# Kernel tuning notes

Measured on AMD Instinct MI355X. Metric: run time of the kernel, lower is better.

The kernel has to match this reference:

```python
import jax, jax.numpy as jnp
import numpy as np

EMB = 128
BINS = 32
CUT = 5.0
NLAYER = 5
NHID = 4  # extra hidden linears in edge MLP (hidden_dim_list has 5 entries total)
N_NODES = 50000
N_EDGES = 800000
N_GRAPH = 256
NODE_CLASS = 100


def setup_inputs() -> dict:
    key = jax.random.key(0)
    ks = jax.random.split(key, 20)
    s = 0.02
    inp = {
        'z': jax.random.randint(ks[0], (N_NODES,), 0, NODE_CLASS),
        'pos': jax.random.normal(ks[1], (N_NODES, 3), dtype=jnp.float32) * 3.0,
        'batch': jnp.sort(jax.random.randint(ks[2], (N_NODES,), 0, N_GRAPH)),
        'edge_index': jax.random.randint(ks[3], (2, N_EDGES), 0, N_NODES),
        # parameters
        'atom_table': jax.random.normal(ks[4], (NODE_CLASS, EMB), dtype=jnp.float32) * s,
        'atom_w': jax.random.normal(ks[5], (EMB, EMB), dtype=jnp.float32) * s,
        'atom_b': jnp.zeros((EMB,), jnp.float32),
        'edge_emb_w': jax.random.normal(ks[6], (BINS, EMB), dtype=jnp.float32) * s,
        'edge_emb_b': jnp.zeros((EMB,), jnp.float32),
        'edge_w0': jax.random.normal(ks[7], (NLAYER, 3 * EMB, EMB), dtype=jnp.float32) * s,
        'edge_b0': jnp.zeros((NLAYER, EMB), jnp.float32),
        'edge_w': jax.random.normal(ks[8], (NLAYER, NHID, EMB, EMB), dtype=jnp.float32) * s,
        'edge_b': jnp.zeros((NLAYER, NHID, EMB), jnp.float32),
        'node_w': jax.random.normal(ks[9], (NLAYER, EMB, EMB), dtype=jnp.float32) * s,
        'node_b': jnp.zeros((NLAYER, EMB), jnp.float32),
        'out_w': jax.random.normal(ks[10], (EMB, 1), dtype=jnp.float32) * s,
        'out_b': jnp.zeros((1,), jnp.float32),
    }
    return inp


def reference(z, pos, batch, edge_index, atom_table, atom_w, atom_b,
              edge_emb_w, edge_emb_b, edge_w0, edge_b0, edge_w, edge_b,
              node_w, node_b, out_w, out_b):
    silu = jax.nn.silu
    row, col = edge_index[0], edge_index[1]

    # atom embedding + linear
    h_node = atom_table[z] @ atom_w + atom_b  # [N, EMB]

    # edge distances -> gaussian basis expansion (linear spacing, log_base=1.0)
    d = jnp.linalg.norm(pos[row] - pos[col], axis=-1)  # [E]
    mu = jnp.linspace(0.0, CUT, BINS, dtype=jnp.float32)
    sigma = CUT / BINS
    basis = jnp.exp(-0.5 * ((d[:, None] - mu) / sigma) ** 2)  # [E, BINS]
    h_edge = basis @ edge_emb_w + edge_emb_b  # [E, EMB]

    # message passing layers
    for l in range(NLAYER):
        m = jnp.concatenate([h_edge, h_node[row], h_node[col]], axis=-1)  # [E, 3*EMB]
        m = silu(m @ edge_w0[l] + edge_b0[l])
        for k in range(NHID):
            m = silu(m @ edge_w[l, k] + edge_b[l, k])
        h_edge = h_edge + m  # residual edge update
        agg = jax.ops.segment_sum(h_edge, row, num_segments=N_NODES)  # [N, EMB]
        h_node = h_node + silu(agg @ node_w[l] + node_b[l])  # residual node update

    # scatter-mean graph pool
    sums = jax.ops.segment_sum(h_node, batch, num_segments=N_GRAPH)
    cnt = jax.ops.segment_sum(jnp.ones((h_node.shape[0],), h_node.dtype), batch, num_segments=N_GRAPH)
    h_graph = sums / jnp.clip(cnt, 1.0)[:, None]

    return h_graph @ out_w + out_b  # [N_GRAPH, 1]
```

## Files before the change

### kernel.cpp

```cpp
#include <hip/hip_runtime.h>

#define EMB      128
#define N_NODES_ 50000
#define N_EDGES_ 800000
#define N_GRAPH_ 256
#define NLAYER_  5

#define WP_ATOM  573440
#define WP_NODE0 589824
#define WP_EMB   671744
#define WP_TOTAL 675840

typedef short short8 __attribute__((ext_vector_type(8)));
typedef float floatx4 __attribute__((ext_vector_type(4)));

__device__ __forceinline__ float silu_f(float x) {
    return __fdividef(x, 1.0f + __expf(-x));
}
__device__ __forceinline__ float bf2f(unsigned short h) {
    return __uint_as_float(((unsigned)h) << 16);
}
__device__ __forceinline__ unsigned short f2bf(float f) {
    unsigned u = __float_as_uint(f);
    unsigned r = 0x7FFFu + ((u >> 16) & 1u);
    return (unsigned short)((u + r) >> 16);
}

#if defined(__has_builtin)
#if __has_builtin(__builtin_amdgcn_cvt_pk_bf16_f32)
#define HAVE_PK_BF16 1
#endif
#endif
#ifdef HAVE_PK_BF16
typedef __bf16 bf16x2 __attribute__((ext_vector_type(2)));
__device__ __forceinline__ unsigned f2bf_pk(float a, float b) {
    bf16x2 v = __builtin_amdgcn_cvt_pk_bf16_f32(a, b);
    unsigned u;
    __builtin_memcpy(&u, &v, 4);
    return u;
}
#else
__device__ __forceinline__ unsigned f2bf_pk(float a, float b) {
    return (unsigned)f2bf(a) | ((unsigned)f2bf(b) << 16);
}
#endif

__device__ __forceinline__ void wave_lds_fence() {
    __builtin_amdgcn_fence(__ATOMIC_ACQ_REL, "wavefront");
    __builtin_amdgcn_wave_barrier();
}

__global__ __launch_bounds__(256) void hist_kernel(
    const int* __restrict__ row, int* __restrict__ hist)
{
    const int e = blockIdx.x * 256 + threadIdx.x;
    if (e < N_EDGES_) atomicAdd(&hist[row[e]], 1);
}

__global__ __launch_bounds__(256) void scan_kernel(
    const int* __restrict__ hist, int* __restrict__ cursor)
{
    __shared__ int ssum[256];
    const int tid = threadIdx.x;
    const int chunk = (N_NODES_ + 255) / 256;
    const int base = tid * chunk;
    int s = 0;
    for (int i = 0; i < chunk; ++i) {
        const int idx = base + i;
        if (idx < N_NODES_) s += hist[idx];
    }
    ssum[tid] = s;
    __syncthreads();
    for (int off = 1; off < 256; off <<= 1) {
        const int t2 = (tid >= off) ? ssum[tid - off] : 0;
        __syncthreads();
        ssum[tid] += t2;
        __syncthreads();
    }
    int run = ssum[tid] - s;
    for (int i = 0; i < chunk; ++i) {
        const int idx = base + i;
        if (idx < N_NODES_) { cursor[idx] = run; run += hist[idx]; }
    }
}

__global__ __launch_bounds__(256) void scatter_kernel(
    const int* __restrict__ row, const int* __restrict__ col,
    int* __restrict__ cursor, int* __restrict__ row_s, int* __restrict__ col_s)
{
    const int e = blockIdx.x * 256 + threadIdx.x;
    if (e >= N_EDGES_) return;
    const int r = row[e];
    const int p = atomicAdd(&cursor[r], 1);
    row_s[p] = r;
    col_s[p] = col[e];
}

__global__ __launch_bounds__(256) void pack_w_kernel(
    const float* __restrict__ edge_w0, const float* __restrict__ edge_w,
    const float* __restrict__ atom_w, const float* __restrict__ node_w,
    const float* __restrict__ edge_emb_w,
    unsigned short* __restrict__ Wp)
{
    const int bid = blockIdx.x;
    int Kb, t;
    const float* src;
    unsigned short* dst;
    if (bid < 200) {
        const int l = bid / 40, r = bid % 40, s = r / 8;
        t = r % 8;
        Kb = (s == 0) ? 12 : 4;
        src = (s == 0) ? edge_w0 + (size_t)l * 384 * 128
                       : edge_w + ((size_t)l * 4 + (s - 1)) * 128 * 128;
        dst = Wp + (size_t)l * 114688 + ((s == 0) ? 0 : (49152 + (s - 1) * 16384))
            + (size_t)t * Kb * 512;
    } else if (bid < 208) {
        t = bid - 200; Kb = 4; src = atom_w;
        dst = Wp + WP_ATOM + (size_t)t * Kb * 512;
    } else if (bid < 248) {
        const int l = (bid - 208) >> 3; t = (bid - 208) & 7; Kb = 4;
        src = node_w + (size_t)l * 128 * 128;
        dst = Wp + WP_NODE0 + (size_t)l * 16384 + (size_t)t * Kb * 512;
    } else {
        t = bid - 248; Kb = 1; src = edge_emb_w;
        dst = Wp + WP_EMB + (size_t)t * 512;
    }
    const int n = Kb * 512;
    for (int p = threadIdx.x; p < n; p += 256) {
        const int j = p & 7, lane = (p >> 3) & 63, kb = p >> 9;
        const int k  = kb * 32 + ((lane >> 4) << 3) + j;
        const int nn = t * 16 + (lane & 15);
        dst[p] = f2bf(src[(size_t)k * 128 + nn]);
    }
}

__global__ __launch_bounds__(256, 4) void edge_mlp_csr_kernel(
    const unsigned short* __restrict__ h_node_bf, unsigned short* __restrict__ h_edge,
    const int* __restrict__ row_s, const int* __restrict__ col_s,
    const unsigned short* __restrict__ Wp,
    const float* __restrict__ b0, const float* __restrict__ bh)
{
    __shared__ __align__(16) unsigned short P[2][64][136];

    const int tid  = threadIdx.x;
    const int e0   = blockIdx.x * 64;
    const int lane = tid & 63;
    const int wv   = tid >> 6;
    const int lr   = lane & 15;
    const int lg   = lane >> 4;
    const int nt0  = 2 * wv, nt1 = nt0 + 1;

    int eoff[4], roff[4], coff[4];
#pragma unroll
    for (int et = 0; et < 4; ++et) {
        const int e = e0 + et * 16 + lr;
        eoff[et] = e * 128 + lg * 8;
        roff[et] = row_s[e] * 128 + lg * 8;
        coff[et] = col_s[e] * 128 + lg * 8;
    }

    floatx4 acc0[4], acc1[4];

    {
        const float4 bv0 = *(const float4*)&b0[nt0 * 16 + lg * 4];
        const float4 bv1 = *(const float4*)&b0[nt1 * 16 + lg * 4];
#pragma unroll
        for (int et = 0; et < 4; ++et) {
            acc0[et] = (floatx4){bv0.x, bv0.y, bv0.z, bv0.w};
            acc1[et] = (floatx4){bv1.x, bv1.y, bv1.z, bv1.w};
        }
        const unsigned short* aptr0 = Wp + ((size_t)(nt0 * 12) * 64 + lane) * 8;
        const unsigned short* aptr1 = Wp + ((size_t)(nt1 * 12) * 64 + lane) * 8;
#pragma unroll
        for (int kb = 0; kb < 12; ++kb) {
            const short8 wf0 = *(const short8*)(aptr0 + (size_t)kb * 512);
            const short8 wf1 = *(const short8*)(aptr1 + (size_t)kb * 512);
            const int off = (kb & 3) * 32;
#pragma unroll
            for (int et = 0; et < 4; ++et) {
                const unsigned short* src =
                    (kb < 4) ? (h_edge + eoff[et])
                  : (kb < 8) ? (h_node_bf + roff[et])
                             : (h_node_bf + coff[et]);
                const short8 mf = *(const short8*)(src + off);
                acc0[et] = __builtin_amdgcn_mfma_f32_16x16x32_bf16(wf0, mf, acc0[et], 0, 0, 0);
                acc1[et] = __builtin_amdgcn_mfma_f32_16x16x32_bf16(wf1, mf, acc1[et], 0, 0, 0);
            }
        }
#pragma unroll
        for (int et = 0; et < 4; ++et) {
            uint2 p0, p1;
            p0.x = f2bf_pk(silu_f(acc0[et][0]), silu_f(acc0[et][1]));
            p0.y = f2bf_pk(silu_f(acc0[et][2]), silu_f(acc0[et][3]));
            p1.x = f2bf_pk(silu_f(acc1[et][0]), silu_f(acc1[et][1]));
            p1.y = f2bf_pk(silu_f(acc1[et][2]), silu_f(acc1[et][3]));
            *(uint2*)&P[0][et * 16 + lr][nt0 * 16 + lg * 4] = p0;
            *(uint2*)&P[0][et * 16 + lr][nt1 * 16 + lg * 4] = p1;
        }
    }
    __syncthreads();

#pragma unroll 1
    for (int s = 1; s < 5; ++s) {
        const int inb  = (s - 1) & 1;
        const int outb = s & 1;
        const unsigned short* __restrict__ Ws = Wp + 49152 + (size_t)(s - 1) * 16384;
        const float* __restrict__ bias = bh + (size_t)(s - 1) * 128;

        const float4 bv0 = *(const float4*)&bias[nt0 * 16 + lg * 4];
        const float4 bv1 = *(const float4*)&bias[nt1 * 16 + lg * 4];
#pragma unroll
        for (int et = 0; et < 4; ++et) {
            acc0[et] = (floatx4){bv0.x, bv0.y, bv0.z, bv0.w};
            acc1[et] = (floatx4){bv1.x, bv1.y, bv1.z, bv1.w};
        }
        const unsigned short* aptr0 = Ws + ((size_t)(nt0 * 4) * 64 + lane) * 8;
        const unsigned short* aptr1 = Ws + ((size_t)(nt1 * 4) * 64 + lane) * 8;
#pragma unroll 2
        for (int kb = 0; kb < 4; ++kb) {
            const short8 wf0 = *(const short8*)(aptr0 + (size_t)kb * 512);
            const short8 wf1 = *(const short8*)(aptr1 + (size_t)kb * 512);
#pragma unroll
            for (int et = 0; et < 4; ++et) {
                const short8 mf = *(const short8*)&P[inb][et * 16 + lr][kb * 32 + lg * 8];
                acc0[et] = __builtin_amdgcn_mfma_f32_16x16x32_bf16(wf0, mf, acc0[et], 0, 0, 0);
                acc1[et] = __builtin_amdgcn_mfma_f32_16x16x32_bf16(wf1, mf, acc1[et], 0, 0, 0);
            }
        }
        if (s < 4) {
#pragma unroll
            for (int et = 0; et < 4; ++et) {
                uint2 p0, p1;
                p0.x = f2bf_pk(silu_f(acc0[et][0]), silu_f(acc0[et][1]));
                p0.y = f2bf_pk(silu_f(acc0[et][2]), silu_f(acc0[et][3]));
                p1.x = f2bf_pk(silu_f(acc1[et][0]), silu_f(acc1[et][1]));
                p1.y = f2bf_pk(silu_f(acc1[et][2]), silu_f(acc1[et][3]));
                *(uint2*)&P[outb][et * 16 + lr][nt0 * 16 + lg * 4] = p0;
                *(uint2*)&P[outb][et * 16 + lr][nt1 * 16 + lg * 4] = p1;
            }
            __syncthreads();
        } else {
#pragma unroll
            for (int et = 0; et < 4; ++et) {
                unsigned short* erow = h_edge + (size_t)(e0 + et * 16 + lr) * 128;
                const uint2 d0 = *(const uint2*)(erow + nt0 * 16 + lg * 4);
                const uint2 d1 = *(const uint2*)(erow + nt1 * 16 + lg * 4);
                float x0 = silu_f(acc0[et][0]) + bf2f((unsigned short)(d0.x & 0xFFFF));
                float x1 = silu_f(acc0[et][1]) + bf2f((unsigned short)(d0.x >> 16));
                float x2 = silu_f(acc0[et][2]) + bf2f((unsigned short)(d0.y & 0xFFFF));
                float x3 = silu_f(acc0[et][3]) + bf2f((unsigned short)(d0.y >> 16));
                float y0 = silu_f(acc1[et][0]) + bf2f((unsigned short)(d1.x & 0xFFFF));
                float y1 = silu_f(acc1[et][1]) + bf2f((unsigned short)(d1.x >> 16));
                float y2 = silu_f(acc1[et][2]) + bf2f((unsigned short)(d1.y & 0xFFFF));
                float y3 = silu_f(acc1[et][3]) + bf2f((unsigned short)(d1.y >> 16));
                uint2 o0, o1;
                o0.x = f2bf_pk(x0, x1); o0.y = f2bf_pk(x2, x3);
                o1.x = f2bf_pk(y0, y1); o1.y = f2bf_pk(y2, y3);
                *(uint2*)(erow + nt0 * 16 + lg * 4) = o0;
                *(uint2*)(erow + nt1 * 16 + lg * 4) = o1;
            }
        }
    }
}

__global__ __launch_bounds__(256, 4) void node_agg_gemm_kernel(
    const unsigned short* __restrict__ h_edge,
    const int* __restrict__ hist, const int* __restrict__ cur_end,
    const unsigned short* __restrict__ Wpm, const float* __restrict__ bias,
    unsigned short* __restrict__ h_node_bf, int N)
{
    __shared__ __align__(16) unsigned short B[64][136];
    const int tid  = threadIdx.x;
    const int lane = tid & 63;
    const int wv   = tid >> 6;
    const int n0   = blockIdx.x * 64;

    {
        const int t = tid >> 2, q = tid & 3;
        const int n = n0 + t;
        float a[32];
#pragma unroll
        for (int j = 0; j < 32; ++j) a[j] = 0.f;
        if (n < N) {
            const int e_end = cur_end[n];
            const int e_beg = e_end - hist[n];
            for (int e = e_beg; e < e_end; ++e) {
                const unsigned short* p = &h_edge[(size_t)e * 128 + q * 32];
#pragma unroll
                for (int g = 0; g < 4; ++g) {
                    const short8 v = *(const short8*)(p + g * 8);
#pragma unroll
                    for (int j = 0; j < 8; ++j)
                        a[g * 8 + j] += bf2f((unsigned short)v[j]);
                }
            }
        }
#pragma unroll
        for (int g = 0; g < 4; ++g) {
            uint4 pk;
            pk.x = f2bf_pk(a[g * 8 + 0], a[g * 8 + 1]);
            pk.y = f2bf_pk(a[g * 8 + 2], a[g * 8 + 3]);
            pk.z = f2bf_pk(a[g * 8 + 4], a[g * 8 + 5]);
            pk.w = f2bf_pk(a[g * 8 + 6], a[g * 8 + 7]);
            *(uint4*)&B[t][q * 32 + g * 8] = pk;
        }
    }
    wave_lds_fence();

    const int lr = lane & 15, lg = lane >> 4;
    floatx4 acc[8];
#pragma unroll
    for (int nt = 0; nt < 8; ++nt) {
        const float4 bv = *(const float4*)&bias[nt * 16 + lg * 4];
        acc[nt] = (floatx4){bv.x, bv.y, bv.z, bv.w};
    }
    const unsigned short* brow = &B[wv * 16 + lr][0];
#pragma unroll 2
    for (int kb = 0; kb < 4; ++kb) {
        const short8 mf = *(const short8*)(brow + kb * 32 + lg * 8);
#pragma unroll
        for (int nt = 0; nt < 8; ++nt) {
            const short8 wf = *(const short8*)(Wpm + ((size_t)(nt * 4 + kb) * 64 + lane) * 8);
            acc[nt] = __builtin_amdgcn_mfma_f32_16x16x32_bf16(wf, mf, acc[nt], 0, 0, 0);
        }
    }
    const int node = n0 + wv * 16 + lr;
    if (node < N) {
        unsigned short* drow = &h_node_bf[(size_t)node * 128];
#pragma unroll
        for (int nt = 0; nt < 8; ++nt) {
            float x0 = silu_f(acc[nt][0]), x1 = silu_f(acc[nt][1]);
            float x2 = silu_f(acc[nt][2]), x3 = silu_f(acc[nt][3]);
            unsigned short* p = drow + nt * 16 + lg * 4;
            const uint2 d = *(const uint2*)p;
            x0 += bf2f((unsigned short)(d.x & 0xFFFF));
            x1 += bf2f((unsigned short)(d.x >> 16));
            x2 += bf2f((unsigned short)(d.y & 0xFFFF));
            x3 += bf2f((unsigned short)(d.y >> 16));
            uint2 o;
            o.x = f2bf_pk(x0, x1);
            o.y = f2bf_pk(x2, x3);
            *(uint2*)p = o;
        }
    }
}

__global__ __launch_bounds__(256, 4) void atom_gemm_mfma_kernel(
    const float* __restrict__ src, const int* __restrict__ gidx,
    const unsigned short* __restrict__ Wpm, const float* __restrict__ bias,
    unsigned short* __restrict__ dst, int N)
{
    __shared__ __align__(16) unsigned short B[64][136];
    const int tid  = threadIdx.x;
    const int lane = tid & 63;
    const int wv   = tid >> 6;
    const int n0   = blockIdx.x * 64;

    {
        const int t = tid >> 2, q = tid & 3;
        const int node = n0 + t;
        const float* srow = src;
        if (node < N) srow = &src[(size_t)gidx[node] * 128];
#pragma unroll
        for (int i = 0; i < 4; ++i) {
            const int k8 = (q + 4 * i) << 3;
            uint4 pk = make_uint4(0, 0, 0, 0);
            if (node < N) {
                const float4 f0 = *(const float4*)(srow + k8);
                const float4 f1 = *(const float4*)(srow + k8 + 4);
                pk.x = f2bf_pk(f0.x, f0.y);
                pk.y = f2bf_pk(f0.z, f0.w);
                pk.z = f2bf_pk(f1.x, f1.y);
                pk.w = f2bf_pk(f1.z, f1.w);
            }
            *(uint4*)&B[t][k8] = pk;
        }
    }
    wave_lds_fence();

    const int lr = lane & 15, lg = lane >> 4;
    floatx4 acc[8];
#pragma unroll
    for (int nt = 0; nt < 8; ++nt) {
        const float4 bv = *(const float4*)&bias[nt * 16 + lg * 4];
        acc[nt] = (floatx4){bv.x, bv.y, bv.z, bv.w};
    }
    const unsigned short* brow = &B[wv * 16 + lr][0];
#pragma unroll 2
    for (int kb = 0; kb < 4; ++kb) {
        const short8 mf = *(const short8*)(brow + kb * 32 + lg * 8);
#pragma unroll
        for (int nt = 0; nt < 8; ++nt) {
            const short8 wf = *(const short8*)(Wpm + ((size_t)(nt * 4 + kb) * 64 + lane) * 8);
            acc[nt] = __builtin_amdgcn_mfma_f32_16x16x32_bf16(wf, mf, acc[nt], 0, 0, 0);
        }
    }
    const int node = n0 + wv * 16 + lr;
    if (node < N) {
        unsigned short* drow = &dst[(size_t)node * 128];
#pragma unroll
        for (int nt = 0; nt < 8; ++nt) {
            uint2 o;
            o.x = f2bf_pk(acc[nt][0], acc[nt][1]);
            o.y = f2bf_pk(acc[nt][2], acc[nt][3]);
            *(uint2*)(drow + nt * 16 + lg * 4) = o;
        }
    }
}

__global__ __launch_bounds__(256, 4) void edge_embed_mfma_kernel(
    const float* __restrict__ pos, const int* __restrict__ row, const int* __restrict__ col,
    const unsigned short* __restrict__ Wpe, const float* __restrict__ bemb,
    unsigned short* __restrict__ h_edge)
{
    __shared__ __align__(16) unsigned short Bas[64][40];
    const int tid  = threadIdx.x;
    const int lane = tid & 63;
    const int wv   = tid >> 6;
    const int e0   = blockIdx.x * 64;

    {
        const int t = tid >> 2, q = tid & 3;
        const int rr = row[e0 + t], cc = col[e0 + t];
        const float dx = pos[rr * 3 + 0] - pos[cc * 3 + 0];
        const float dy = pos[rr * 3 + 1] - pos[cc * 3 + 1];
        const float dz = pos[rr * 3 + 2] - pos[cc * 3 + 2];
        const float d = sqrtf(dx * dx + dy * dy + dz * dz);
        const float invs = 32.0f / 5.0f;
        float e[8];
#pragma unroll
        for (int j = 0; j < 8; ++j) {
            const float mu = (float)(q * 8 + j) * (5.0f / 31.0f);
            const float tt = (d - mu) * invs;
            e[j] = __expf(-0.5f * tt * tt);
        }
        uint4 pk;
        pk.x = f2bf_pk(e[0], e[1]);
        pk.y = f2bf_pk(e[2], e[3]);
        pk.z = f2bf_pk(e[4], e[5]);
        pk.w = f2bf_pk(e[6], e[7]);
        *(uint4*)&Bas[t][q * 8] = pk;
    }
    wave_lds_fence();

    const int lr = lane & 15, lg = lane >> 4;
    floatx4 acc[8];
#pragma unroll
    for (int nt = 0; nt < 8; ++nt) {
        const float4 bv = *(const float4*)&bemb[nt * 16 + lg * 4];
        acc[nt] = (floatx4){bv.x, bv.y, bv.z, bv.w};
    }
    const short8 mf = *(const short8*)&Bas[wv * 16 + lr][lg * 8];
#pragma unroll
    for (int nt = 0; nt < 8; ++nt) {
        const short8 wf = *(const short8*)(Wpe + ((size_t)nt * 64 + lane) * 8);
        acc[nt] = __builtin_amdgcn_mfma_f32_16x16x32_bf16(wf, mf, acc[nt], 0, 0, 0);
    }
    unsigned short* erow = &h_edge[(size_t)(e0 + wv * 16 + lr) * 128];
#pragma unroll
    for (int nt = 0; nt < 8; ++nt) {
        uint2 o;
        o.x = f2bf_pk(acc[nt][0], acc[nt][1]);
        o.y = f2bf_pk(acc[nt][2], acc[nt][3]);
        *(uint2*)(erow + nt * 16 + lg * 4) = o;
    }
}

__global__ __launch_bounds__(128) void pool_kernel(
    const unsigned short* __restrict__ h_node_bf, const int* __restrict__ batch,
    float* __restrict__ sums, float* __restrict__ cnt, int N)
{
    __shared__ int bb[256];
    const int tid = threadIdx.x;
    const int n0 = blockIdx.x * 256;
    for (int idx = tid; idx < 256; idx += 128) {
        int n = n0 + idx;
        bb[idx] = (n < N) ? batch[n] : -1;
    }
    __syncthreads();
    int cur = bb[0];
    float run = 0.f, runc = 0.f;
    for (int i = 0; i < 256; ++i) {
        const int b = bb[i];
        if (b < 0) break;
        if (b != cur) {
            atomicAdd(&sums[(size_t)cur * 128 + tid], run);
            if (tid == 0) atomicAdd(&cnt[cur], runc);
            run = 0.f; runc = 0.f; cur = b;
        }
        run += bf2f(h_node_bf[(size_t)(n0 + i) * 128 + tid]);
        runc += 1.f;
    }
    atomicAdd(&sums[(size_t)cur * 128 + tid], run);
    if (tid == 0) atomicAdd(&cnt[cur], runc);
}

__global__ __launch_bounds__(256) void final_kernel(
    const float* __restrict__ sums, const float* __restrict__ cnt,
    const float* __restrict__ out_w, const float* __restrict__ out_b,
    float* __restrict__ out)
{
    const int g = threadIdx.x;
    const float c = fmaxf(cnt[g], 1.0f);
    float acc = 0.f;
    for (int jj = 0; jj < 128; ++jj) acc = fmaf(sums[(size_t)g * 128 + jj], out_w[jj], acc);
    out[g] = acc / c + out_b[0];
}

__global__ void zero_out_kernel(float* out, int n) {
    int i = blockIdx.x * 256 + threadIdx.x;
    if (i < n) out[i] = 0.f;
}


extern "C" void kernel_launch(void* const* d_in, const int* in_sizes, int n_in,
                              void* d_out, int out_size, void* d_ws, size_t ws_size,
                              hipStream_t stream)
{
    const int*   z          = (const int*)  d_in[0];
    const float* pos        = (const float*)d_in[1];
    const int*   batch      = (const int*)  d_in[2];
    const int*   eidx       = (const int*)  d_in[3];
    const float* atom_table = (const float*)d_in[4];
    const float* atom_w     = (const float*)d_in[5];
    const float* atom_b     = (const float*)d_in[6];
    const float* edge_emb_w = (const float*)d_in[7];
    const float* edge_emb_b = (const float*)d_in[8];
    const float* edge_w0    = (const float*)d_in[9];
    const float* edge_b0    = (const float*)d_in[10];
    const float* edge_w     = (const float*)d_in[11];
    const float* edge_b     = (const float*)d_in[12];
    const float* node_w     = (const float*)d_in[13];
    const float* node_b     = (const float*)d_in[14];
    const float* out_w      = (const float*)d_in[15];
    const float* out_b      = (const float*)d_in[16];
    const int* row = eidx;
    const int* col = eidx + N_EDGES_;

    float* aggb = (float*)d_ws;
    float* sums = aggb + (size_t)N_NODES_ * EMB;
    float* cnt  = sums + (size_t)N_GRAPH_ * EMB;
    unsigned short* h_node_bf = (unsigned short*)(cnt + N_GRAPH_);
    unsigned short* h_edge    = h_node_bf + (size_t)N_NODES_ * EMB;
    unsigned short* Wp        = h_edge + (size_t)N_EDGES_ * EMB;
    int* hist   = (int*)(Wp + WP_TOTAL);
    int* cursor = hist + N_NODES_;
    int* row_s  = cursor + N_NODES_;
    int* col_s  = row_s + N_EDGES_;

    const size_t need = ((size_t)(N_NODES_ * EMB + N_GRAPH_ * EMB + N_GRAPH_)) * 4
                      + ((size_t)N_NODES_ * EMB + (size_t)N_EDGES_ * EMB + (size_t)WP_TOTAL) * 2
                      + ((size_t)N_NODES_ * 2 + (size_t)N_EDGES_ * 2) * 4;

    if (ws_size < need) {
        zero_out_kernel<<<1, 256, 0, stream>>>((float*)d_out, N_GRAPH_);
        return;
    }

    const int grid_rows64 = (N_NODES_ + 63) / 64;

    (void)hipMemsetAsync(hist, 0, N_NODES_ * sizeof(int), stream);
    hist_kernel<<<(N_EDGES_ + 255) / 256, 256, 0, stream>>>(row, hist);
    scan_kernel<<<1, 256, 0, stream>>>(hist, cursor);
    scatter_kernel<<<(N_EDGES_ + 255) / 256, 256, 0, stream>>>(row, col, cursor, row_s, col_s);

    pack_w_kernel<<<256, 256, 0, stream>>>(edge_w0, edge_w, atom_w, node_w, edge_emb_w, Wp);

    atom_gemm_mfma_kernel<<<grid_rows64, 256, 0, stream>>>(
        atom_table, z, Wp + WP_ATOM, atom_b, h_node_bf, N_NODES_);
    edge_embed_mfma_kernel<<<N_EDGES_ / 64, 256, 0, stream>>>(
        pos, row_s, col_s, Wp + WP_EMB, edge_emb_b, h_edge);

    for (int l = 0; l < NLAYER_; ++l) {
        edge_mlp_csr_kernel<<<N_EDGES_ / 64, 256, 0, stream>>>(
            h_node_bf, h_edge, row_s, col_s,
            Wp + (size_t)l * 114688,
            edge_b0 + (size_t)l * 128, edge_b + (size_t)l * 4 * 128);
        node_agg_gemm_kernel<<<grid_rows64, 256, 0, stream>>>(
            h_edge, hist, cursor,
            Wp + WP_NODE0 + (size_t)l * 16384, node_b + (size_t)l * 128,
            h_node_bf, N_NODES_);
    }

    (void)hipMemsetAsync(sums, 0, ((size_t)N_GRAPH_ * EMB + N_GRAPH_) * sizeof(float), stream);
    pool_kernel<<<(N_NODES_ + 255) / 256, 128, 0, stream>>>(h_node_bf, batch, sums, cnt, N_NODES_);
    final_kernel<<<1, 256, 0, stream>>>(sums, cnt, out_w, out_b, (float*)d_out);
}
```

Before: 2.796 ms.

## Stage edge MLP gathers into swizzled LDS via direct global-to-LDS loads

The first edge-MLP layer used to read h_edge, h_node[row] and h_node[col] straight from global memory inside the MFMA loop. It now stages 64-row tiles into two XOR-swizzled LDS buffers with global_load_lds, prefetching the next segment while the current one is multiplied. The final residual is now done through LDS with coalesced 16-byte stores, and an extra occupancy level is requested through launch_bounds. The aim is to hide gather latency and cut redundant scattered global reads, at the cost of more synchronisation and hand-written vmcnt waits that must line up with the outstanding loads.

```diff
diff --git a/kernel.cpp b/kernel.cpp
--- a/kernel.cpp
+++ b/kernel.cpp
@@ -48,6 +48,13 @@
 __device__ __forceinline__ void wave_lds_fence() {
     __builtin_amdgcn_fence(__ATOMIC_ACQ_REL, "wavefront");
     __builtin_amdgcn_wave_barrier();
+}
+
+__device__ __forceinline__ void gload_lds16(const unsigned short* g, unsigned short* l) {
+    __builtin_amdgcn_global_load_lds(
+        (const __attribute__((address_space(1))) void*)g,
+        (__attribute__((address_space(3))) void*)l,
+        16, 0, 0);
 }
 
 __global__ __launch_bounds__(256) void hist_kernel(
@@ -134,13 +141,14 @@
     }
 }
 
-__global__ __launch_bounds__(256, 4) void edge_mlp_csr_kernel(
+__global__ __launch_bounds__(256, 5) void edge_mlp_csr_kernel(
     const unsigned short* __restrict__ h_node_bf, unsigned short* __restrict__ h_edge,
     const int* __restrict__ row_s, const int* __restrict__ col_s,
     const unsigned short* __restrict__ Wp,
     const float* __restrict__ b0, const float* __restrict__ bh)
 {
-    __shared__ __align__(16) unsigned short P[2][64][136];
+    __shared__ __align__(16) unsigned short Xs[8192];
+    __shared__ __align__(16) unsigned short Ys[8192];
 
     const int tid  = threadIdx.x;
     const int e0   = blockIdx.x * 64;
@@ -150,17 +158,32 @@
     const int lg   = lane >> 4;
     const int nt0  = 2 * wv, nt1 = nt0 + 1;
 
-    int eoff[4], roff[4], coff[4];
-#pragma unroll
-    for (int et = 0; et < 4; ++et) {
-        const int e = e0 + et * 16 + lr;
-        eoff[et] = e * 128 + lg * 8;
-        roff[et] = row_s[e] * 128 + lg * 8;
-        coff[et] = col_s[e] * 128 + lg * 8;
+    const int t_ = tid >> 2, q_ = tid & 3;
+    short8 he_reg[4];
+#pragma unroll
+    for (int i = 0; i < 4; ++i)
+        he_reg[i] = *(const short8*)&h_edge[(size_t)(e0 + t_) * 128 + (q_ + 4 * i) * 8];
+
+    const int srow = 16 * wv + lg;
+#pragma unroll
+    for (int j = 0; j < 4; ++j) {
+        const int r = srow + 4 * j;
+        const int c = lr ^ (r & 7);
+        gload_lds16(h_edge + (size_t)(e0 + r) * 128 + c * 8,
+                    &Xs[(16 * wv + 4 * j) * 128]);
+    }
+    int cnode[4];
+#pragma unroll
+    for (int j = 0; j < 4; ++j) {
+        const int r = srow + 4 * j;
+        const int c = lr ^ (r & 7);
+        const int nd = row_s[e0 + r];
+        cnode[j] = col_s[e0 + r];
+        gload_lds16(h_node_bf + (size_t)nd * 128 + c * 8,
+                    &Ys[(16 * wv + 4 * j) * 128]);
     }
 
     floatx4 acc0[4], acc1[4];
-
     {
         const float4 bv0 = *(const float4*)&b0[nt0 * 16 + lg * 4];
         const float4 bv1 = *(const float4*)&b0[nt1 * 16 + lg * 4];
@@ -169,97 +192,137 @@
             acc0[et] = (floatx4){bv0.x, bv0.y, bv0.z, bv0.w};
             acc1[et] = (floatx4){bv1.x, bv1.y, bv1.z, bv1.w};
         }
-        const unsigned short* aptr0 = Wp + ((size_t)(nt0 * 12) * 64 + lane) * 8;
-        const unsigned short* aptr1 = Wp + ((size_t)(nt1 * 12) * 64 + lane) * 8;
-#pragma unroll
-        for (int kb = 0; kb < 12; ++kb) {
-            const short8 wf0 = *(const short8*)(aptr0 + (size_t)kb * 512);
-            const short8 wf1 = *(const short8*)(aptr1 + (size_t)kb * 512);
-            const int off = (kb & 3) * 32;
+    }
+    const unsigned short* aptr0 = Wp + ((size_t)(nt0 * 12) * 64 + lane) * 8;
+    const unsigned short* aptr1 = Wp + ((size_t)(nt1 * 12) * 64 + lane) * 8;
+
+    asm volatile("s_waitcnt vmcnt(4)" ::: "memory");
+    __syncthreads();
+
+#pragma unroll 2
+    for (int kk = 0; kk < 4; ++kk) {
+        const short8 wf0 = *(const short8*)(aptr0 + (size_t)kk * 512);
+        const short8 wf1 = *(const short8*)(aptr1 + (size_t)kk * 512);
+#pragma unroll
+        for (int et = 0; et < 4; ++et) {
+            const int r = et * 16 + lr;
+            const short8 mf = *(const short8*)&Xs[r * 128 + (((kk * 4 + lg) ^ (r & 7)) << 3)];
+            acc0[et] = __builtin_amdgcn_mfma_f32_16x16x32_bf16(wf0, mf, acc0[et], 0, 0, 0);
+            acc1[et] = __builtin_amdgcn_mfma_f32_16x16x32_bf16(wf1, mf, acc1[et], 0, 0, 0);
+        }
+    }
+    asm volatile("s_waitcnt vmcnt(0)" ::: "memory");
+    __syncthreads();
+
+#pragma unroll
+    for (int j = 0; j < 4; ++j) {
+        const int r = srow + 4 * j;
+        const int c = lr ^ (r & 7);
+        gload_lds16(h_node_bf + (size_t)cnode[j] * 128 + c * 8,
+                    &Xs[(16 * wv + 4 * j) * 128]);
+    }
+
+#pragma unroll 2
+    for (int kk = 0; kk < 4; ++kk) {
+        const short8 wf0 = *(const short8*)(aptr0 + (size_t)(kk + 4) * 512);
+        const short8 wf1 = *(const short8*)(aptr1 + (size_t)(kk + 4) * 512);
+#pragma unroll
+        for (int et = 0; et < 4; ++et) {
+            const int r = et * 16 + lr;
+            const short8 mf = *(const short8*)&Ys[r * 128 + (((kk * 4 + lg) ^ (r & 7)) << 3)];
+            acc0[et] = __builtin_amdgcn_mfma_f32_16x16x32_bf16(wf0, mf, acc0[et], 0, 0, 0);
+            acc1[et] = __builtin_amdgcn_mfma_f32_16x16x32_bf16(wf1, mf, acc1[et], 0, 0, 0);
+        }
+    }
+    asm volatile("s_waitcnt vmcnt(0)" ::: "memory");
+    __syncthreads();
+
+#pragma unroll 2
+    for (int kk = 0; kk < 4; ++kk) {
+        const short8 wf0 = *(const short8*)(aptr0 + (size_t)(kk + 8) * 512);
+        const short8 wf1 = *(const short8*)(aptr1 + (size_t)(kk + 8) * 512);
+#pragma unroll
+        for (int et = 0; et < 4; ++et) {
+            const int r = et * 16 + lr;
+            const short8 mf = *(const short8*)&Xs[r * 128 + (((kk * 4 + lg) ^ (r & 7)) << 3)];
+            acc0[et] = __builtin_amdgcn_mfma_f32_16x16x32_bf16(wf0, mf, acc0[et], 0, 0, 0);
+            acc1[et] = __builtin_amdgcn_mfma_f32_16x16x32_bf16(wf1, mf, acc1[et], 0, 0, 0);
+        }
+    }
+#pragma unroll
+    for (int et = 0; et < 4; ++et) {
+        const int r = et * 16 + lr;
+        uint2 p0, p1;
+        p0.x = f2bf_pk(silu_f(acc0[et][0]), silu_f(acc0[et][1]));
+        p0.y = f2bf_pk(silu_f(acc0[et][2]), silu_f(acc0[et][3]));
+        p1.x = f2bf_pk(silu_f(acc1[et][0]), silu_f(acc1[et][1]));
+        p1.y = f2bf_pk(silu_f(acc1[et][2]), silu_f(acc1[et][3]));
+        const int c0 = (2 * nt0 + (lg >> 1)) ^ (r & 7);
+        const int c1 = (2 * nt1 + (lg >> 1)) ^ (r & 7);
+        *(uint2*)&Ys[r * 128 + c0 * 8 + (lg & 1) * 4] = p0;
+        *(uint2*)&Ys[r * 128 + c1 * 8 + (lg & 1) * 4] = p1;
+    }
+    __syncthreads();
+
+#pragma unroll 1
+    for (int s = 1; s < 5; ++s) {
+        const unsigned short* bin = (s & 1) ? Ys : Xs;
+        unsigned short* bout      = (s & 1) ? Xs : Ys;
+        const unsigned short* __restrict__ Ws = Wp + 49152 + (size_t)(s - 1) * 16384;
+        const float* __restrict__ bias = bh + (size_t)(s - 1) * 128;
+
+        const float4 bv0 = *(const float4*)&bias[nt0 * 16 + lg * 4];
+        const float4 bv1 = *(const float4*)&bias[nt1 * 16 + lg * 4];
+#pragma unroll
+        for (int et = 0; et < 4; ++et) {
+            acc0[et] = (floatx4){bv0.x, bv0.y, bv0.z, bv0.w};
+            acc1[et] = (floatx4){bv1.x, bv1.y, bv1.z, bv1.w};
+        }
+        const unsigned short* ap0 = Ws + ((size_t)(nt0 * 4) * 64 + lane) * 8;
+        const unsigned short* ap1 = Ws + ((size_t)(nt1 * 4) * 64 + lane) * 8;
+#pragma unroll 2
+        for (int kk = 0; kk < 4; ++kk) {
+            const short8 wf0 = *(const short8*)(ap0 + (size_t)kk * 512);
+            const short8 wf1 = *(const short8*)(ap1 + (size_t)kk * 512);
 #pragma unroll
             for (int et = 0; et < 4; ++et) {
-                const unsigned short* src =
-                    (kb < 4) ? (h_edge + eoff[et])
-                  : (kb < 8) ? (h_node_bf + roff[et])
-                             : (h_node_bf + coff[et]);
-                const short8 mf = *(const short8*)(src + off);
+                const int r = et * 16 + lr;
+                const short8 mf = *(const short8*)&bin[r * 128 + (((kk * 4 + lg) ^ (r & 7)) << 3)];
                 acc0[et] = __builtin_amdgcn_mfma_f32_16x16x32_bf16(wf0, mf, acc0[et], 0, 0, 0);
                 acc1[et] = __builtin_amdgcn_mfma_f32_16x16x32_bf16(wf1, mf, acc1[et], 0, 0, 0);
             }
         }
 #pragma unroll
         for (int et = 0; et < 4; ++et) {
+            const int r = et * 16 + lr;
             uint2 p0, p1;
             p0.x = f2bf_pk(silu_f(acc0[et][0]), silu_f(acc0[et][1]));
             p0.y = f2bf_pk(silu_f(acc0[et][2]), silu_f(acc0[et][3]));
             p1.x = f2bf_pk(silu_f(acc1[et][0]), silu_f(acc1[et][1]));
             p1.y = f2bf_pk(silu_f(acc1[et][2]), silu_f(acc1[et][3]));
-            *(uint2*)&P[0][et * 16 + lr][nt0 * 16 + lg * 4] = p0;
-            *(uint2*)&P[0][et * 16 + lr][nt1 * 16 + lg * 4] = p1;
-        }
-    }
-    __syncthreads();
-
-#pragma unroll 1
-    for (int s = 1; s < 5; ++s) {
-        const int inb  = (s - 1) & 1;
-        const int outb = s & 1;
-        const unsigned short* __restrict__ Ws = Wp + 49152 + (size_t)(s - 1) * 16384;
-        const float* __restrict__ bias = bh + (size_t)(s - 1) * 128;
-
-        const float4 bv0 = *(const float4*)&bias[nt0 * 16 + lg * 4];
-        const float4 bv1 = *(const float4*)&bias[nt1 * 16 + lg * 4];
-#pragma unroll
-        for (int et = 0; et < 4; ++et) {
-            acc0[et] = (floatx4){bv0.x, bv0.y, bv0.z, bv0.w};
-            acc1[et] = (floatx4){bv1.x, bv1.y, bv1.z, bv1.w};
-        }
-        const unsigned short* aptr0 = Ws + ((size_t)(nt0 * 4) * 64 + lane) * 8;
-        const unsigned short* aptr1 = Ws + ((size_t)(nt1 * 4) * 64 + lane) * 8;
-#pragma unroll 2
-        for (int kb = 0; kb < 4; ++kb) {
-            const short8 wf0 = *(const short8*)(aptr0 + (size_t)kb * 512);
-            const short8 wf1 = *(const short8*)(aptr1 + (size_t)kb * 512);
-#pragma unroll
-            for (int et = 0; et < 4; ++et) {
-                const short8 mf = *(const short8*)&P[inb][et * 16 + lr][kb * 32 + lg * 8];
-                acc0[et] = __builtin_amdgcn_mfma_f32_16x16x32_bf16(wf0, mf, acc0[et], 0, 0, 0);
-                acc1[et] = __builtin_amdgcn_mfma_f32_16x16x32_bf16(wf1, mf, acc1[et], 0, 0, 0);
-            }
-        }
-        if (s < 4) {
-#pragma unroll
-            for (int et = 0; et < 4; ++et) {
-                uint2 p0, p1;
-                p0.x = f2bf_pk(silu_f(acc0[et][0]), silu_f(acc0[et][1]));
-                p0.y = f2bf_pk(silu_f(acc0[et][2]), silu_f(acc0[et][3]));
-                p1.x = f2bf_pk(silu_f(acc1[et][0]), silu_f(acc1[et][1]));
-                p1.y = f2bf_pk(silu_f(acc1[et][2]), silu_f(acc1[et][3]));
-                *(uint2*)&P[outb][et * 16 + lr][nt0 * 16 + lg * 4] = p0;
-                *(uint2*)&P[outb][et * 16 + lr][nt1 * 16 + lg * 4] = p1;
-            }
-            __syncthreads();
-        } else {
-#pragma unroll
-            for (int et = 0; et < 4; ++et) {
-                unsigned short* erow = h_edge + (size_t)(e0 + et * 16 + lr) * 128;
-                const uint2 d0 = *(const uint2*)(erow + nt0 * 16 + lg * 4);
-                const uint2 d1 = *(const uint2*)(erow + nt1 * 16 + lg * 4);
-                float x0 = silu_f(acc0[et][0]) + bf2f((unsigned short)(d0.x & 0xFFFF));
-                float x1 = silu_f(acc0[et][1]) + bf2f((unsigned short)(d0.x >> 16));
-                float x2 = silu_f(acc0[et][2]) + bf2f((unsigned short)(d0.y & 0xFFFF));
-                float x3 = silu_f(acc0[et][3]) + bf2f((unsigned short)(d0.y >> 16));
-                float y0 = silu_f(acc1[et][0]) + bf2f((unsigned short)(d1.x & 0xFFFF));
-                float y1 = silu_f(acc1[et][1]) + bf2f((unsigned short)(d1.x >> 16));
-                float y2 = silu_f(acc1[et][2]) + bf2f((unsigned short)(d1.y & 0xFFFF));
-                float y3 = silu_f(acc1[et][3]) + bf2f((unsigned short)(d1.y >> 16));
-                uint2 o0, o1;
-                o0.x = f2bf_pk(x0, x1); o0.y = f2bf_pk(x2, x3);
-                o1.x = f2bf_pk(y0, y1); o1.y = f2bf_pk(y2, y3);
-                *(uint2*)(erow + nt0 * 16 + lg * 4) = o0;
-                *(uint2*)(erow + nt1 * 16 + lg * 4) = o1;
-            }
-        }
+            const int c0 = (2 * nt0 + (lg >> 1)) ^ (r & 7);
+            const int c1 = (2 * nt1 + (lg >> 1)) ^ (r & 7);
+            *(uint2*)&bout[r * 128 + c0 * 8 + (lg & 1) * 4] = p0;
+            *(uint2*)&bout[r * 128 + c1 * 8 + (lg & 1) * 4] = p1;
+        }
+        __syncthreads();
+    }
+
+#pragma unroll
+    for (int i = 0; i < 4; ++i) {
+        const int ch = q_ + 4 * i;
+        const short8 mv = *(const short8*)&Ys[t_ * 128 + ((ch ^ (t_ & 7)) << 3)];
+        const short8 ov = he_reg[i];
+        float he[8];
+#pragma unroll
+        for (int j = 0; j < 8; ++j)
+            he[j] = bf2f((unsigned short)ov[j]) + bf2f((unsigned short)mv[j]);
+        uint4 sv;
+        sv.x = f2bf_pk(he[0], he[1]);
+        sv.y = f2bf_pk(he[2], he[3]);
+        sv.z = f2bf_pk(he[4], he[5]);
+        sv.w = f2bf_pk(he[6], he[7]);
+        *(uint4*)(h_edge + (size_t)(e0 + t_) * 128 + ch * 8) = sv;
     }
 }
 
```

After: 2.556 ms. 8.6% less time.
